# Optimization experiments

Hardware: AMD Instinct MI355X
Metric: run time of the kernel (lower is better)

The kernel has to match this reference:

```python
import jax, jax.numpy as jnp
import numpy as np

NUM_HEADS = 16
NUM_GQA_GROUPS = 4
HEAD_DIM = 128
TOTAL_TOKENS = 4096
NUM_SEQS = 8
SCALE = HEAD_DIM ** -0.5


def setup_inputs() -> dict:
    key = jax.random.key(0)
    kq, kk, kv, kc = jax.random.split(key, 4)
    query = jax.random.normal(kq, (TOTAL_TOKENS, NUM_HEADS, HEAD_DIM), dtype=jnp.float32)
    k = jax.random.normal(kk, (TOTAL_TOKENS, NUM_GQA_GROUPS, HEAD_DIM), dtype=jnp.float32)
    v = jax.random.normal(kv, (TOTAL_TOKENS, NUM_GQA_GROUPS, HEAD_DIM), dtype=jnp.float32)
    # cu_seqlens: sorted prefix boundaries, pinned to 0 and TOTAL_TOKENS
    inner = jnp.sort(jax.random.randint(kc, (NUM_SEQS - 1,), 1, TOTAL_TOKENS, dtype=jnp.int32))
    cu_seqlens = jnp.concatenate([
        jnp.zeros((1,), jnp.int32), inner,
        jnp.full((1,), TOTAL_TOKENS, jnp.int32)])
    return {"query": query, "key": k, "value": v, "cu_seqlens": cu_seqlens}


def reference(query, key, value, cu_seqlens):
    """Packed varlen (thd) causal attention with GQA, fused via a segment mask.

    query: [T, H, D]; key/value: [T, G, D]; cu_seqlens: [B+1] int32.
    Returns [T, H, D] (same layout the torch thd path concatenates back to).
    """
    T, H, D = query.shape
    ratio = H // key.shape[1]
    if ratio > 1:  # GQA: repeat kv heads to match query heads
        key = jnp.repeat(key, ratio, axis=1)
        value = jnp.repeat(value, ratio, axis=1)

    pos = jnp.arange(T, dtype=jnp.int32)
    # segment id of each packed token: cu[j] <= i < cu[j+1]
    seg = jnp.searchsorted(cu_seqlens, pos, side="right") - 1
    # within-segment causal mask (global causal == local causal inside a segment)
    mask = (seg[:, None] == seg[None, :]) & (pos[:, None] >= pos[None, :])  # [T, T]

    scores = jnp.einsum("qhd,khd->hqk", query, key) * SCALE  # [H, T, T]
    scores = jnp.where(mask[None], scores, -jnp.inf)
    probs = jax.nn.softmax(scores, axis=-1)
    out = jnp.einsum("hqk,khd->qhd", probs, value)  # [T, H, D]
    return out
```

## Files before the change

### kernel.cpp

```cpp
#include <hip/hip_runtime.h>
#include <hip/hip_bf16.h>


#define T_TOK 4096
#define NH    16
#define NG    4
#define HD    128
#define NCU   9

#define ML_OFF 33554432l

typedef short          short8_t __attribute__((ext_vector_type(8)));
typedef float          float4_t __attribute__((ext_vector_type(4)));
typedef unsigned int   uint2_t  __attribute__((ext_vector_type(2)));
typedef unsigned short ushort;

static __device__ inline unsigned pack2(float a, float b) {
    __hip_bfloat162 h = __float22bfloat162_rn(make_float2(a, b));
    union { __hip_bfloat162 h; unsigned u; } c; c.h = h;
    return c.u;
}
static __device__ inline short8_t cvt8(float4_t lo, float4_t hi) {
    union { unsigned u[4]; short8_t s; } r;
    r.u[0] = pack2(lo[0], lo[1]); r.u[1] = pack2(lo[2], lo[3]);
    r.u[2] = pack2(hi[0], hi[1]); r.u[3] = pack2(hi[2], hi[3]);
    return r.s;
}

template <bool CHUNKED>
__global__ __launch_bounds__(512) void attn_fwd_k(
    const float* __restrict__ Q,
    const float* __restrict__ K,
    const float* __restrict__ V,
    const int*   __restrict__ cu,
    float*       __restrict__ O,
    float*       __restrict__ WS)
{
    __shared__ __align__(16) unsigned char smem[58368];
    ushort (*Ks)[32][136]   = (ushort (*)[32][136])smem;
    ushort (*Vt)[128][40]   = (ushort (*)[128][40])(smem + 17408);
    ushort (*pb)[2][16][40] = (ushort (*)[2][16][40])(smem + 37888);

    const int qtile = (int)gridDim.x - 1 - (int)blockIdx.x;
    const int g     = blockIdx.y;
    const int cz    = CHUNKED ? (int)blockIdx.z : 0;
    const int tid   = threadIdx.x;
    const int wave  = tid >> 6;
    const int split = wave >> 2;
    const int hw    = wave & 3;
    const int lane  = tid & 63;
    const int h     = g * 4 + hw;
    const int col   = lane & 15;
    const int quad  = lane >> 4;

    const int qbase = qtile * 32;
    const int qq[2] = { qbase + col, qbase + 16 + col };

    int seg_start[2] = {0, 0}, seg0 = 0;
    #pragma unroll
    for (int j = 1; j < NCU; ++j) {
        int cj = cu[j];
        if (cj <= qq[0])  seg_start[0] = cj;
        if (cj <= qq[1])  seg_start[1] = cj;
        if (cj <= qbase)  seg0         = cj;
    }
    const int k0       = seg0 & ~31;
    const int nblk_tot = (qbase + 32 - k0) >> 5;
    const int nc       = CHUNKED ? ((nblk_tot + 31) >> 5) : 1;
    if (CHUNKED && cz >= nc) return;
    int nblk = nblk_tot - (cz << 5);
    if (CHUNKED && nblk > 32) nblk = 32;
    const int nb0    = (nblk + 1) >> 1;
    const int kstart = k0 + (cz << 10) + split * nb0 * 32;

    short8_t qf[2][4];
    #pragma unroll
    for (int tt = 0; tt < 2; ++tt) {
        const float* qp = Q + ((long)qq[tt] * NH + h) * HD + quad * 8;
        #pragma unroll
        for (int c = 0; c < 4; ++c)
            qf[tt][c] = cvt8(*(const float4_t*)(qp + c * 32),
                             *(const float4_t*)(qp + c * 32 + 4));
    }

    float4_t oacc[2][8];
    #pragma unroll
    for (int tt = 0; tt < 2; ++tt)
        #pragma unroll
        for (int dt = 0; dt < 8; ++dt) oacc[tt][dt] = (float4_t){0.f, 0.f, 0.f, 0.f};

    float m_run[2] = {-10000.0f, -10000.0f};
    float l_run[2] = {0.0f, 0.0f};
    const float c_scale = 0.08838834764831845f * 1.4426950408889634f;

    const int stid = tid & 255;
    const int ki  = stid >> 3;
    const int ch  = (stid & 7) * 16;
    const int kp2 = (stid & 15) * 2;
    const int dc  = (stid >> 4) * 8;

    float4_t kreg[4], vreg[4];
    {
        int key = kstart + ki; if (key > T_TOK - 1) key = T_TOK - 1;
        const float* kp = K + ((long)key * NG + g) * HD + ch;
        kreg[0] = *(const float4_t*)kp;       kreg[1] = *(const float4_t*)(kp + 4);
        kreg[2] = *(const float4_t*)(kp + 8); kreg[3] = *(const float4_t*)(kp + 12);
        int key0 = kstart + kp2;     if (key0 > T_TOK - 1) key0 = T_TOK - 1;
        int key1 = kstart + kp2 + 1; if (key1 > T_TOK - 1) key1 = T_TOK - 1;
        const float* v0 = V + ((long)key0 * NG + g) * HD + dc;
        const float* v1 = V + ((long)key1 * NG + g) * HD + dc;
        vreg[0] = *(const float4_t*)v0; vreg[1] = *(const float4_t*)(v0 + 4);
        vreg[2] = *(const float4_t*)v1; vreg[3] = *(const float4_t*)(v1 + 4);
    }

    for (int it = 0; it < nb0; ++it) {
        const int kb = kstart + it * 32;
        __syncthreads();

        *(short8_t*)&Ks[split][ki][ch]     = cvt8(kreg[0], kreg[1]);
        *(short8_t*)&Ks[split][ki][ch + 8] = cvt8(kreg[2], kreg[3]);
        #pragma unroll
        for (int d = 0; d < 4; ++d) {
            *(unsigned*)&Vt[split][dc + d][kp2]     = pack2(vreg[0][d], vreg[2][d]);
            *(unsigned*)&Vt[split][dc + 4 + d][kp2] = pack2(vreg[1][d], vreg[3][d]);
        }
        __syncthreads();

        {
            int nb = kb + 32;
            int key = nb + ki; if (key > T_TOK - 1) key = T_TOK - 1;
            const float* kp = K + ((long)key * NG + g) * HD + ch;
            kreg[0] = *(const float4_t*)kp;       kreg[1] = *(const float4_t*)(kp + 4);
            kreg[2] = *(const float4_t*)(kp + 8); kreg[3] = *(const float4_t*)(kp + 12);
            int key0 = nb + kp2;     if (key0 > T_TOK - 1) key0 = T_TOK - 1;
            int key1 = nb + kp2 + 1; if (key1 > T_TOK - 1) key1 = T_TOK - 1;
            const float* v0 = V + ((long)key0 * NG + g) * HD + dc;
            const float* v1 = V + ((long)key1 * NG + g) * HD + dc;
            vreg[0] = *(const float4_t*)v0; vreg[1] = *(const float4_t*)(v0 + 4);
            vreg[2] = *(const float4_t*)v1; vreg[3] = *(const float4_t*)(v1 + 4);
        }

        float4_t st[2][2];
        #pragma unroll
        for (int tt = 0; tt < 2; ++tt)
            #pragma unroll
            for (int t = 0; t < 2; ++t) st[tt][t] = (float4_t){0.f, 0.f, 0.f, 0.f};
        #pragma unroll
        for (int c = 0; c < 4; ++c) {
            short8_t kf0 = *(const short8_t*)&Ks[split][col][c * 32 + quad * 8];
            short8_t kf1 = *(const short8_t*)&Ks[split][16 + col][c * 32 + quad * 8];
            st[0][0] = __builtin_amdgcn_mfma_f32_16x16x32_bf16(kf0, qf[0][c], st[0][0], 0, 0, 0);
            st[0][1] = __builtin_amdgcn_mfma_f32_16x16x32_bf16(kf1, qf[0][c], st[0][1], 0, 0, 0);
            st[1][0] = __builtin_amdgcn_mfma_f32_16x16x32_bf16(kf0, qf[1][c], st[1][0], 0, 0, 0);
            st[1][1] = __builtin_amdgcn_mfma_f32_16x16x32_bf16(kf1, qf[1][c], st[1][1], 0, 0, 0);
        }

        #pragma unroll
        for (int tt = 0; tt < 2; ++tt) {
            float tv[8];
            #pragma unroll
            for (int t = 0; t < 2; ++t)
                #pragma unroll
                for (int r = 0; r < 4; ++r) {
                    int key = kb + 16 * t + quad * 4 + r;
                    bool valid = (key <= qq[tt]) && (key >= seg_start[tt]);
                    tv[t * 4 + r] = valid ? st[tt][t][r] * c_scale : -30000.0f;
                }
            float tmax = tv[0];
            #pragma unroll
            for (int i = 1; i < 8; ++i) tmax = fmaxf(tmax, tv[i]);
            tmax = fmaxf(tmax, __shfl_xor(tmax, 16));
            tmax = fmaxf(tmax, __shfl_xor(tmax, 32));
            const float m_new = fmaxf(m_run[tt], tmax);
            float p[8], ps = 0.f;
            #pragma unroll
            for (int i = 0; i < 8; ++i) { p[i] = __builtin_exp2f(tv[i] - m_new); ps += p[i]; }
            ps += __shfl_xor(ps, 16);
            ps += __shfl_xor(ps, 32);
            if (__any(tmax > m_run[tt])) {
                const float alpha = __builtin_exp2f(m_run[tt] - m_new);
                l_run[tt] = l_run[tt] * alpha + ps;
                m_run[tt] = m_new;
                #pragma unroll
                for (int dt = 0; dt < 8; ++dt) oacc[tt][dt] *= alpha;
            } else {
                l_run[tt] += ps;
            }

            uint2_t w0; w0.x = pack2(p[0], p[1]); w0.y = pack2(p[2], p[3]);
            uint2_t w1; w1.x = pack2(p[4], p[5]); w1.y = pack2(p[6], p[7]);
            *(uint2_t*)&pb[wave][tt][col][quad * 4]      = w0;
            *(uint2_t*)&pb[wave][tt][col][16 + quad * 4] = w1;
        }
        short8_t pf0 = *(const short8_t*)&pb[wave][0][col][quad * 8];
        short8_t pf1 = *(const short8_t*)&pb[wave][1][col][quad * 8];

        #pragma unroll
        for (int dt = 0; dt < 8; ++dt) {
            short8_t vf = *(const short8_t*)&Vt[split][dt * 16 + col][quad * 8];
            oacc[0][dt] = __builtin_amdgcn_mfma_f32_16x16x32_bf16(vf, pf0, oacc[0][dt], 0, 0, 0);
            oacc[1][dt] = __builtin_amdgcn_mfma_f32_16x16x32_bf16(vf, pf1, oacc[1][dt], 0, 0, 0);
        }
    }

    float* Ob = (float*)smem;
    float* cm = (float*)(smem + 34816);
    float* cl = (float*)(smem + 35840);
    #pragma unroll
    for (int tt = 0; tt < 2; ++tt) {
        __syncthreads();
        if (split == 1) {
            if (quad == 0) { cm[hw * 16 + col] = m_run[tt]; cl[hw * 16 + col] = l_run[tt]; }
            float* ob = Ob + (hw * 16 + col) * 132;
            #pragma unroll
            for (int dt = 0; dt < 8; ++dt)
                *(float4_t*)(ob + dt * 16 + quad * 4) = oacc[tt][dt];
        }
        __syncthreads();
        if (split == 0) {
            const float m1 = cm[hw * 16 + col], l1 = cl[hw * 16 + col];
            const float m  = fmaxf(m_run[tt], m1);
            const float a0 = __builtin_exp2f(m_run[tt] - m);
            const float a1 = __builtin_exp2f(m1 - m);
            const float* ob = Ob + (hw * 16 + col) * 132;
            #pragma unroll
            for (int dt = 0; dt < 8; ++dt) {
                float4_t o1 = *(const float4_t*)(ob + dt * 16 + quad * 4);
                oacc[tt][dt] = oacc[tt][dt] * a0 + o1 * a1;
            }
            l_run[tt] = l_run[tt] * a0 + l1 * a1;
            m_run[tt] = m;
        }
    }

    if (split == 0) {
        if (!CHUNKED || nc == 1) {
            #pragma unroll
            for (int tt = 0; tt < 2; ++tt) {
                const float inv_l = 1.0f / l_run[tt];
                float* op = O + ((long)qq[tt] * NH + h) * HD + quad * 4;
                #pragma unroll
                for (int dt = 0; dt < 8; ++dt) {
                    float4_t ov;
                    #pragma unroll
                    for (int r = 0; r < 4; ++r) ov[r] = oacc[tt][dt][r] * inv_l;
                    *(float4_t*)(op + dt * 16) = ov;
                }
            }
        } else {
            const long slot = ((long)(qtile * 4 + g)) * 4 + cz;
            #pragma unroll
            for (int tt = 0; tt < 2; ++tt) {
                const int ql = tt * 16 + col;
                if (quad == 0) {
                    float* mlp = WS + ML_OFF + (slot * 128 + hw * 32 + ql) * 2;
                    mlp[0] = m_run[tt];
                    mlp[1] = l_run[tt];
                }
                float* op = WS + (slot * 128 + hw * 32 + ql) * 128 + quad * 4;
                #pragma unroll
                for (int dt = 0; dt < 8; ++dt)
                    *(float4_t*)(op + dt * 16) = oacc[tt][dt];
            }
        }
    }
}

__global__ __launch_bounds__(256) void attn_merge(
    const int*   __restrict__ cu,
    const float* __restrict__ WS,
    float*       __restrict__ O)
{
    const int tile  = blockIdx.x;
    const int g     = blockIdx.y;
    const int qbase = tile * 32;
    int seg0 = 0;
    #pragma unroll
    for (int j = 1; j < NCU; ++j) { int cj = cu[j]; if (cj <= qbase) seg0 = cj; }
    const int k0       = seg0 & ~31;
    const int nblk_tot = (qbase + 32 - k0) >> 5;
    const int nc       = (nblk_tot + 31) >> 5;
    if (nc <= 1) return;

    const int tid  = threadIdx.x;
    const int pair = tid >> 1;
    const int half = tid & 1;
    const int hw   = pair >> 5;
    const int q    = pair & 31;

    float m = -30000.0f, l = 0.0f;
    float4_t acc[16];
    #pragma unroll
    for (int i = 0; i < 16; ++i) acc[i] = (float4_t){0.f, 0.f, 0.f, 0.f};

    for (int c = 0; c < nc; ++c) {
        const long slot = ((long)(tile * 4 + g)) * 4 + c;
        const float* mlp = WS + ML_OFF + (slot * 128 + pair) * 2;
        const float mc = mlp[0], lc = mlp[1];
        const float mn = fmaxf(m, mc);
        const float a0 = __builtin_exp2f(m - mn);
        const float a1 = __builtin_exp2f(mc - mn);
        l = l * a0 + lc * a1;
        const float* op = WS + (slot * 128 + pair) * 128 + half * 64;
        #pragma unroll
        for (int i = 0; i < 16; ++i) {
            float4_t v = *(const float4_t*)(op + i * 4);
            acc[i] = acc[i] * a0 + v * a1;
        }
        m = mn;
    }
    const float inv = 1.0f / l;
    float* o = O + ((long)(qbase + q) * NH + g * 4 + hw) * HD + half * 64;
    #pragma unroll
    for (int i = 0; i < 16; ++i)
        *(float4_t*)(o + i * 4) = acc[i] * inv;
}

extern "C" void kernel_launch(void* const* d_in, const int* in_sizes, int n_in,
                              void* d_out, int out_size, void* d_ws, size_t ws_size,
                              hipStream_t stream) {
    const float* Q  = (const float*)d_in[0];
    const float* K  = (const float*)d_in[1];
    const float* V  = (const float*)d_in[2];
    const int*   cu = (const int*)d_in[3];
    float*       O  = (float*)d_out;
    const size_t need = (size_t)(33554432l + 524288l) * sizeof(float);
    if (d_ws != nullptr && ws_size >= need) {
        attn_fwd_k<true><<<dim3(T_TOK / 32, NG, 4), 512, 0, stream>>>(
            Q, K, V, cu, O, (float*)d_ws);
        attn_merge<<<dim3(T_TOK / 32, NG), 256, 0, stream>>>(
            cu, (const float*)d_ws, O);
    } else {
        attn_fwd_k<false><<<dim3(T_TOK / 32, NG), 512, 0, stream>>>(
            Q, K, V, cu, O, nullptr);
    }
}
```

Measured before the change: 213.9 us.

## Replace chunked grid with persistent kernel pulling longest-first work queue

Adds a single-block prepass that computes each query tile's KV block count, sorts tiles by work descending, and builds a queue containing only the needed (tile, group, chunk) entries. A persistent 512-block kernel then pops entries with an atomic counter, so blocks with no work are never launched and the heaviest tiles are scheduled first. This targets launch overhead for empty chunks and tail imbalance. In exchange it adds an extra tiny kernel launch, per-item atomics and barriers, and a dependence on the queue counter being reset on every call.

Result: faster. 188.2 us (-12.0%).

```diff
diff --git a/kernel.cpp b/kernel.cpp
--- a/kernel.cpp
+++ b/kernel.cpp
@@ -7,8 +7,10 @@
 #define NG    4
 #define HD    128
 #define NCU   9
+#define NTILE 128
 
 #define ML_OFF 33554432l
+#define Q_OFF  (ML_OFF + 524288l)
 
 typedef short          short8_t __attribute__((ext_vector_type(8)));
 typedef float          float4_t __attribute__((ext_vector_type(4)));
@@ -28,22 +30,16 @@
 }
 
 template <bool CHUNKED>
-__global__ __launch_bounds__(512) void attn_fwd_k(
-    const float* __restrict__ Q,
-    const float* __restrict__ K,
-    const float* __restrict__ V,
-    const int*   __restrict__ cu,
-    float*       __restrict__ O,
-    float*       __restrict__ WS)
+static __device__ __forceinline__ void attn_tile_body(
+    const float* __restrict__ Q, const float* __restrict__ K,
+    const float* __restrict__ V, const int* __restrict__ cu,
+    float* __restrict__ O, float* __restrict__ WS,
+    unsigned char* smem, int qtile, int g, int cz)
 {
-    __shared__ __align__(16) unsigned char smem[58368];
     ushort (*Ks)[32][136]   = (ushort (*)[32][136])smem;
     ushort (*Vt)[128][40]   = (ushort (*)[128][40])(smem + 17408);
     ushort (*pb)[2][16][40] = (ushort (*)[2][16][40])(smem + 37888);
 
-    const int qtile = (int)gridDim.x - 1 - (int)blockIdx.x;
-    const int g     = blockIdx.y;
-    const int cz    = CHUNKED ? (int)blockIdx.z : 0;
     const int tid   = threadIdx.x;
     const int wave  = tid >> 6;
     const int split = wave >> 2;
@@ -266,6 +262,82 @@
     }
 }
 
+__global__ __launch_bounds__(128) void build_queue(
+    const int* __restrict__ cu, int* __restrict__ qwork)
+{
+    __shared__ int nblk_s[NTILE];
+    __shared__ int sortedE[NTILE + 1];
+    const int t = threadIdx.x;
+
+    const int qbase = t * 32;
+    int seg0 = 0;
+    #pragma unroll
+    for (int j = 1; j < NCU; ++j) { int cj = cu[j]; if (cj <= qbase) seg0 = cj; }
+    const int k0   = seg0 & ~31;
+    const int nblk = (qbase + 32 - k0) >> 5;
+    nblk_s[t] = nblk;
+    __syncthreads();
+
+    int r = 0;
+    for (int j = 0; j < NTILE; ++j) {
+        int nj = nblk_s[j];
+        if (nj > nblk || (nj == nblk && j < t)) ++r;
+    }
+    const int nc = (nblk + 31) >> 5;
+    sortedE[r] = 4 * nc;
+    __syncthreads();
+    if (t == 0) {
+        int s = 0;
+        for (int j = 0; j < NTILE; ++j) { int v = sortedE[j]; sortedE[j] = s; s += v; }
+        sortedE[NTILE] = s;
+        qwork[0] = s;
+        qwork[1] = 0;
+    }
+    __syncthreads();
+    int off = 2 + sortedE[r];
+    for (int g = 0; g < NG; ++g)
+        for (int cz = 0; cz < nc; ++cz)
+            qwork[off++] = (t << 4) | (g << 2) | cz;
+}
+
+__global__ __launch_bounds__(512) void attn_fwd_persist(
+    const float* __restrict__ Q,
+    const float* __restrict__ K,
+    const float* __restrict__ V,
+    const int*   __restrict__ cu,
+    float*       __restrict__ O,
+    float*       __restrict__ WS)
+{
+    __shared__ __align__(16) unsigned char smem[58368];
+    __shared__ int pop_s;
+    int* qwork = (int*)(WS + Q_OFF);
+    const int qtotal = qwork[0];
+
+    for (;;) {
+        __syncthreads();
+        if (threadIdx.x == 0) pop_s = atomicAdd(&qwork[1], 1);
+        __syncthreads();
+        const int idx = pop_s;
+        if (idx >= qtotal) return;
+        const int ent = qwork[2 + idx];
+        attn_tile_body<true>(Q, K, V, cu, O, WS, smem,
+                             ent >> 4, (ent >> 2) & 3, ent & 3);
+    }
+}
+
+__global__ __launch_bounds__(512) void attn_fwd_mono(
+    const float* __restrict__ Q,
+    const float* __restrict__ K,
+    const float* __restrict__ V,
+    const int*   __restrict__ cu,
+    float*       __restrict__ O)
+{
+    __shared__ __align__(16) unsigned char smem[58368];
+    attn_tile_body<false>(Q, K, V, cu, O, nullptr, smem,
+                          (int)gridDim.x - 1 - (int)blockIdx.x,
+                          (int)blockIdx.y, 0);
+}
+
 __global__ __launch_bounds__(256) void attn_merge(
     const int*   __restrict__ cu,
     const float* __restrict__ WS,
@@ -324,14 +396,14 @@
     const float* V  = (const float*)d_in[2];
     const int*   cu = (const int*)d_in[3];
     float*       O  = (float*)d_out;
-    const size_t need = (size_t)(33554432l + 524288l) * sizeof(float);
+    const size_t need = (size_t)(33554432l + 524288l + 2056l) * sizeof(float);
     if (d_ws != nullptr && ws_size >= need) {
-        attn_fwd_k<true><<<dim3(T_TOK / 32, NG, 4), 512, 0, stream>>>(
-            Q, K, V, cu, O, (float*)d_ws);
+        float* WS = (float*)d_ws;
+        build_queue<<<1, 128, 0, stream>>>(cu, (int*)(WS + Q_OFF));
+        attn_fwd_persist<<<512, 512, 0, stream>>>(Q, K, V, cu, O, WS);
         attn_merge<<<dim3(T_TOK / 32, NG), 256, 0, stream>>>(
-            cu, (const float*)d_ws, O);
+            cu, (const float*)WS, O);
     } else {
-        attn_fwd_k<false><<<dim3(T_TOK / 32, NG), 512, 0, stream>>>(
-            Q, K, V, cu, O, nullptr);
-    }
-}
+        attn_fwd_mono<<<dim3(T_TOK / 32, NG), 512, 0, stream>>>(Q, K, V, cu, O);
+    }
+}
```
